# Kernel optimization log

Measured on AMD Instinct MI355X. Metric: run time of the kernel, lower is better.

Reference implementation:

```python
import jax, jax.numpy as jnp
import numpy as np


def setup_inputs() -> dict:
    key = jax.random.key(0)
    k = jax.random.split(key, 5)
    B, L, D = 8, 2048, 256  # D = 2*d_model, c_len == q_len == L (required by source's s1 broadcast)
    c = jax.random.normal(k[0], (B, L, D), dtype=jnp.float32)
    q = jax.random.normal(k[1], (B, L, D), dtype=jnp.float32)
    c_weight = jax.random.normal(k[2], (D, 1), dtype=jnp.float32) * 0.05
    q_weight = jax.random.normal(k[3], (D, 1), dtype=jnp.float32) * 0.05
    cq_weight = jax.random.normal(k[4], (1, 1, D), dtype=jnp.float32) * 0.05
    bias = jnp.zeros((1,), dtype=jnp.float32)
    return {"c": c, "q": q, "c_weight": c_weight, "q_weight": q_weight,
            "cq_weight": cq_weight, "bias": bias}


def reference(c, q, c_weight, q_weight, cq_weight, bias):
    # Dropout omitted (identity) for a deterministic reference.
    # s0: [B, c_len, 1] -> broadcasts over q_len
    s0 = jnp.matmul(c, c_weight)                       # [B, L, 1]
    # s1 (faithful to source, which uses c here): [B, 1, c_len]
    s1 = jnp.swapaxes(jnp.matmul(c, q_weight), 1, 2)   # [B, 1, L]
    # s2: elementwise-scaled batched GEMM: [B, c_len, q_len]
    s2 = jnp.matmul(c * cq_weight, jnp.swapaxes(q, 1, 2))
    s = s0 + s1 + s2 + bias                            # broadcast sum + scalar bias
    return s
```

## Files before the change

kernel.cpp:

```cpp
#include <hip/hip_runtime.h>
#include <hip/hip_bf16.h>

#define B_ 8
#define L_ 2048
#define D_ 256

typedef __bf16 bf16x8 __attribute__((ext_vector_type(8)));
typedef float f32x4 __attribute__((ext_vector_type(4)));

static __device__ __forceinline__ unsigned short f2bf(float f) {
    unsigned int u = __builtin_bit_cast(unsigned int, f);
    unsigned int lsb = (u >> 16) & 1u;
    u += 0x7fffu + lsb;
    return (unsigned short)(u >> 16);
}

static __device__ __forceinline__ void gload_lds16(const void* g, void* l) {
    __builtin_amdgcn_global_load_lds(
        (const __attribute__((address_space(1))) unsigned int*)g,
        (__attribute__((address_space(3))) unsigned int*)l, 16, 0, 0);
}

__global__ __launch_bounds__(256) void prep_kernel(
    const float* __restrict__ c, const float* __restrict__ q,
    const float* __restrict__ cw, const float* __restrict__ qw,
    const float* __restrict__ cqw, const float* __restrict__ bias,
    unsigned short* __restrict__ Abf, unsigned short* __restrict__ Qbf,
    float* __restrict__ s0, float* __restrict__ s1)
{
    const int wave = threadIdx.x >> 6;
    const int lane = threadIdx.x & 63;
    const int row  = blockIdx.x * 4 + wave;

    const float4 cv  = *(const float4*)(c   + (size_t)row * D_ + lane * 4);
    const float4 qv  = *(const float4*)(q   + (size_t)row * D_ + lane * 4);
    const float4 wc  = *(const float4*)(cw  + lane * 4);
    const float4 wq  = *(const float4*)(qw  + lane * 4);
    const float4 wcq = *(const float4*)(cqw + lane * 4);

    ushort4 av, qb;
    av.x = f2bf(cv.x * wcq.x); av.y = f2bf(cv.y * wcq.y);
    av.z = f2bf(cv.z * wcq.z); av.w = f2bf(cv.w * wcq.w);
    qb.x = f2bf(qv.x); qb.y = f2bf(qv.y);
    qb.z = f2bf(qv.z); qb.w = f2bf(qv.w);
    *(ushort4*)(Abf + (size_t)row * D_ + lane * 4) = av;
    *(ushort4*)(Qbf + (size_t)row * D_ + lane * 4) = qb;

    float p0 = cv.x * wc.x + cv.y * wc.y + cv.z * wc.z + cv.w * wc.w;
    float p1 = cv.x * wq.x + cv.y * wq.y + cv.z * wq.z + cv.w * wq.w;
    #pragma unroll
    for (int off = 32; off > 0; off >>= 1) {
        p0 += __shfl_down(p0, off);
        p1 += __shfl_down(p1, off);
    }
    if (lane == 0) { s0[row] = p0 + bias[0]; s1[row] = p1; }
}

#define BM 128
#define BN 128
#define BK 32
#define NSTEP (D_ / BK)

__global__ __launch_bounds__(256) void gemm_kernel(
    const unsigned short* __restrict__ A, const unsigned short* __restrict__ Q,
    const float* __restrict__ s0, const float* __restrict__ s1,
    float* __restrict__ out)
{
    __shared__ __align__(16) unsigned short As[3][BM * BK];
    __shared__ __align__(16) unsigned short Qs[3][BM * BK];

    const int tid  = threadIdx.x;
    const int wave = tid >> 6;
    const int lane = tid & 63;

    const int lin = blockIdx.x + (blockIdx.y << 4) + (blockIdx.z << 8);
    const int nl  = ((lin & 7) << 8) | (lin >> 3);
    const int b   = nl >> 8;
    const int brow = ((nl >> 4) & 15) * BM;
    const int bcol = (nl & 15) * BN;

    const unsigned short* Ab = A + ((size_t)b * L_ + brow) * D_;
    const unsigned short* Qb = Q + ((size_t)b * L_ + bcol) * D_;

    const int wr = wave >> 1;
    const int wc = wave & 1;

    const f32x4 zero = {0.f, 0.f, 0.f, 0.f};
    f32x4 acc[4][4];
    #pragma unroll
    for (int m = 0; m < 4; ++m)
        #pragma unroll
        for (int n = 0; n < 4; ++n) acc[m][n] = zero;

    auto stage = [&](int s) {
        const int k0 = s * BK;
        unsigned short* ab = &As[s % 3][0];
        unsigned short* qb = &Qs[s % 3][0];
        #pragma unroll
        for (int i = 0; i < 2; ++i) {
            const int sidx = i * 256 + wave * 64 + lane;
            const int row  = sidx >> 2;
            const int sl   = sidx & 3;
            const int ksrc = k0 + ((sl ^ ((row >> 1) & 3)) << 3);
            const int wbase = (i * 256 + wave * 64) * 8;
            gload_lds16(Ab + (size_t)row * D_ + ksrc, ab + wbase);
            gload_lds16(Qb + (size_t)row * D_ + ksrc, qb + wbase);
        }
    };

    auto compute = [&](int t) {
        const unsigned short* ab = &As[t % 3][0];
        const unsigned short* qb = &Qs[t % 3][0];
        bf16x8 af[4], qf[4];
        #pragma unroll
        for (int m = 0; m < 4; ++m) {
            const int row = wr * 64 + m * 16 + (lane & 15);
            const int idx = row * 32 + (((lane >> 4) ^ ((row >> 1) & 3)) << 3);
            af[m] = *(const bf16x8*)(ab + idx);
        }
        #pragma unroll
        for (int n = 0; n < 4; ++n) {
            const int row = wc * 64 + n * 16 + (lane & 15);
            const int idx = row * 32 + (((lane >> 4) ^ ((row >> 1) & 3)) << 3);
            qf[n] = *(const bf16x8*)(qb + idx);
        }
        __builtin_amdgcn_s_setprio(1);
        #pragma unroll
        for (int m = 0; m < 4; ++m)
            #pragma unroll
            for (int n = 0; n < 4; ++n)
                acc[m][n] = __builtin_amdgcn_mfma_f32_16x16x32_bf16(
                    af[m], qf[n], acc[m][n], 0, 0, 0);
        __builtin_amdgcn_s_setprio(0);
    };

    stage(0);
    stage(1);

#define STEP(T, VM) do {                                        \
        if ((T) + 2 < NSTEP) stage((T) + 2);                    \
        asm volatile("s_waitcnt vmcnt(" #VM ")" ::: "memory");  \
        __builtin_amdgcn_s_barrier();                           \
        asm volatile("" ::: "memory");                          \
        compute(T);                                             \
        asm volatile("" ::: "memory");                          \
        __builtin_amdgcn_s_barrier();                           \
        asm volatile("" ::: "memory");                          \
    } while (0)

    STEP(0, 8); STEP(1, 8); STEP(2, 8); STEP(3, 8);
    STEP(4, 8); STEP(5, 8); STEP(6, 4); STEP(7, 0);
#undef STEP

    const float* s0b = s0 + b * L_ + brow;
    const float* s1b = s1 + b * L_ + bcol;
    float s1v[4];
    #pragma unroll
    for (int n = 0; n < 4; ++n) s1v[n] = s1b[wc * 64 + n * 16 + (lane & 15)];
    float* outb = out + ((size_t)b * L_ + brow) * L_ + bcol;
    #pragma unroll
    for (int m = 0; m < 4; ++m) {
        #pragma unroll
        for (int r = 0; r < 4; ++r) {
            const int i = wr * 64 + m * 16 + (lane >> 4) * 4 + r;
            const float s0v = s0b[i];
            float* orow = outb + (size_t)i * L_;
            #pragma unroll
            for (int n = 0; n < 4; ++n)
                orow[wc * 64 + n * 16 + (lane & 15)] = acc[m][n][r] + s0v + s1v[n];
        }
    }
}

__global__ void naive_kernel(const float* __restrict__ c, const float* __restrict__ q,
                             const float* __restrict__ cw, const float* __restrict__ qw,
                             const float* __restrict__ cqw, const float* __restrict__ bias,
                             float* __restrict__ out)
{
    const size_t total = (size_t)B_ * L_ * L_;
    for (size_t idx = (size_t)blockIdx.x * blockDim.x + threadIdx.x; idx < total;
         idx += (size_t)gridDim.x * blockDim.x) {
        const int b = (int)(idx / ((size_t)L_ * L_));
        const int rem = (int)(idx % ((size_t)L_ * L_));
        const int i = rem / L_, j = rem % L_;
        const float* ci = c + ((size_t)b * L_ + i) * D_;
        const float* cj = c + ((size_t)b * L_ + j) * D_;
        const float* qj = q + ((size_t)b * L_ + j) * D_;
        float acc = bias[0];
        for (int d = 0; d < D_; ++d)
            acc += ci[d] * cw[d] + cj[d] * qw[d] + ci[d] * cqw[d] * qj[d];
        out[idx] = acc;
    }
}

extern "C" void kernel_launch(void* const* d_in, const int* in_sizes, int n_in,
                              void* d_out, int out_size, void* d_ws, size_t ws_size,
                              hipStream_t stream) {
    const float* c    = (const float*)d_in[0];
    const float* q    = (const float*)d_in[1];
    const float* cw   = (const float*)d_in[2];
    const float* qw   = (const float*)d_in[3];
    const float* cqw  = (const float*)d_in[4];
    const float* bias = (const float*)d_in[5];
    float* out = (float*)d_out;

    const size_t bytesA = (size_t)B_ * L_ * D_ * 2;
    const size_t need   = 2 * bytesA + 2 * (size_t)B_ * L_ * 4;

    if (ws_size >= need) {
        unsigned short* Abf = (unsigned short*)d_ws;
        unsigned short* Qbf = (unsigned short*)((char*)d_ws + bytesA);
        float* s0 = (float*)((char*)d_ws + 2 * bytesA);
        float* s1 = s0 + (size_t)B_ * L_;
        prep_kernel<<<B_ * L_ / 4, 256, 0, stream>>>(c, q, cw, qw, cqw, bias,
                                                     Abf, Qbf, s0, s1);
        dim3 grid(L_ / BN, L_ / BM, B_);
        gemm_kernel<<<grid, 256, 0, stream>>>(Abf, Qbf, s0, s1, out);
    } else {
        naive_kernel<<<2048, 256, 0, stream>>>(c, q, cw, qw, cqw, bias, out);
    }
}
```

Baseline: 47.45 us.

## Enlarge GEMM tile to 256x256 with 512 threads and preload bias into accumulators

Doubles the block tile in both dimensions (256x256, 8 waves, each wave owning a 128x64 sub-tile), which halves global/L2 re-reads of the bf16 operands per output. It switches to a 1D grid of 512 blocks with a batch-interleaving swizzle, and initializes accumulators with s0+s1 so the epilogue is a plain store. The trade-offs are more accumulator registers per thread (128 floats) under a 2-blocks-per-CU launch bound, and fewer blocks for the GPU's CUs, which could cause spills or load imbalance.

```diff
diff --git a/kernel.cpp b/kernel.cpp
--- a/kernel.cpp
+++ b/kernel.cpp
@@ -56,12 +56,12 @@
     if (lane == 0) { s0[row] = p0 + bias[0]; s1[row] = p1; }
 }
 
-#define BM 128
-#define BN 128
+#define BM 256
+#define BN 256
 #define BK 32
 #define NSTEP (D_ / BK)
 
-__global__ __launch_bounds__(256) void gemm_kernel(
+__global__ __launch_bounds__(512, 2) void gemm_kernel(
     const unsigned short* __restrict__ A, const unsigned short* __restrict__ Q,
     const float* __restrict__ s0, const float* __restrict__ s1,
     float* __restrict__ out)
@@ -73,24 +73,37 @@
     const int wave = tid >> 6;
     const int lane = tid & 63;
 
-    const int lin = blockIdx.x + (blockIdx.y << 4) + (blockIdx.z << 8);
-    const int nl  = ((lin & 7) << 8) | (lin >> 3);
-    const int b   = nl >> 8;
-    const int brow = ((nl >> 4) & 15) * BM;
-    const int bcol = (nl & 15) * BN;
+    const int beta = blockIdx.x;
+    const int bs   = ((beta & 7) << 6) | (beta >> 3);
+    const int b    = bs >> 6;
+    const int brow = ((bs >> 3) & 7) * BM;
+    const int bcol = (bs & 7) * BN;
 
     const unsigned short* Ab = A + ((size_t)b * L_ + brow) * D_;
     const unsigned short* Qb = Q + ((size_t)b * L_ + bcol) * D_;
 
-    const int wr = wave >> 1;
-    const int wc = wave & 1;
-
-    const f32x4 zero = {0.f, 0.f, 0.f, 0.f};
-    f32x4 acc[4][4];
-    #pragma unroll
-    for (int m = 0; m < 4; ++m)
-        #pragma unroll
-        for (int n = 0; n < 4; ++n) acc[m][n] = zero;
+    const int wr = wave >> 2;
+    const int wc = wave & 3;
+
+    float s0v[8][4];
+    #pragma unroll
+    for (int m = 0; m < 8; ++m)
+        #pragma unroll
+        for (int r = 0; r < 4; ++r)
+            s0v[m][r] = s0[(size_t)b * L_ + brow + wr * 128 + m * 16 + (lane >> 4) * 4 + r];
+    float s1v[4];
+    #pragma unroll
+    for (int n = 0; n < 4; ++n)
+        s1v[n] = s1[(size_t)b * L_ + bcol + wc * 64 + n * 16 + (lane & 15)];
+
+    f32x4 acc[8][4];
+    #pragma unroll
+    for (int m = 0; m < 8; ++m)
+        #pragma unroll
+        for (int n = 0; n < 4; ++n)
+            #pragma unroll
+            for (int r = 0; r < 4; ++r)
+                acc[m][n][r] = s0v[m][r] + s1v[n];
 
     auto stage = [&](int s) {
         const int k0 = s * BK;
@@ -98,11 +111,11 @@
         unsigned short* qb = &Qs[s % 3][0];
         #pragma unroll
         for (int i = 0; i < 2; ++i) {
-            const int sidx = i * 256 + wave * 64 + lane;
+            const int sidx = i * 512 + wave * 64 + lane;
             const int row  = sidx >> 2;
             const int sl   = sidx & 3;
             const int ksrc = k0 + ((sl ^ ((row >> 1) & 3)) << 3);
-            const int wbase = (i * 256 + wave * 64) * 8;
+            const int wbase = (i * 512 + wave * 64) * 8;
             gload_lds16(Ab + (size_t)row * D_ + ksrc, ab + wbase);
             gload_lds16(Qb + (size_t)row * D_ + ksrc, qb + wbase);
         }
@@ -111,10 +124,10 @@
     auto compute = [&](int t) {
         const unsigned short* ab = &As[t % 3][0];
         const unsigned short* qb = &Qs[t % 3][0];
-        bf16x8 af[4], qf[4];
-        #pragma unroll
-        for (int m = 0; m < 4; ++m) {
-            const int row = wr * 64 + m * 16 + (lane & 15);
+        bf16x8 af[8], qf[4];
+        #pragma unroll
+        for (int m = 0; m < 8; ++m) {
+            const int row = wr * 128 + m * 16 + (lane & 15);
             const int idx = row * 32 + (((lane >> 4) ^ ((row >> 1) & 3)) << 3);
             af[m] = *(const bf16x8*)(ab + idx);
         }
@@ -126,7 +139,7 @@
         }
         __builtin_amdgcn_s_setprio(1);
         #pragma unroll
-        for (int m = 0; m < 4; ++m)
+        for (int m = 0; m < 8; ++m)
             #pragma unroll
             for (int n = 0; n < 4; ++n)
                 acc[m][n] = __builtin_amdgcn_mfma_f32_16x16x32_bf16(
@@ -152,22 +165,16 @@
     STEP(4, 8); STEP(5, 8); STEP(6, 4); STEP(7, 0);
 #undef STEP
 
-    const float* s0b = s0 + b * L_ + brow;
-    const float* s1b = s1 + b * L_ + bcol;
-    float s1v[4];
-    #pragma unroll
-    for (int n = 0; n < 4; ++n) s1v[n] = s1b[wc * 64 + n * 16 + (lane & 15)];
     float* outb = out + ((size_t)b * L_ + brow) * L_ + bcol;
     #pragma unroll
-    for (int m = 0; m < 4; ++m) {
+    for (int m = 0; m < 8; ++m) {
         #pragma unroll
         for (int r = 0; r < 4; ++r) {
-            const int i = wr * 64 + m * 16 + (lane >> 4) * 4 + r;
-            const float s0v = s0b[i];
-            float* orow = outb + (size_t)i * L_;
+            const int row = wr * 128 + m * 16 + (lane >> 4) * 4 + r;
+            float* rp = outb + (size_t)row * L_;
             #pragma unroll
             for (int n = 0; n < 4; ++n)
-                orow[wc * 64 + n * 16 + (lane & 15)] = acc[m][n][r] + s0v + s1v[n];
+                rp[wc * 64 + n * 16 + (lane & 15)] = acc[m][n][r];
         }
     }
 }
@@ -214,8 +221,7 @@
         float* s1 = s0 + (size_t)B_ * L_;
         prep_kernel<<<B_ * L_ / 4, 256, 0, stream>>>(c, q, cw, qw, cqw, bias,
                                                      Abf, Qbf, s0, s1);
-        dim3 grid(L_ / BN, L_ / BM, B_);
-        gemm_kernel<<<grid, 256, 0, stream>>>(Abf, Qbf, s0, s1, out);
+        gemm_kernel<<<dim3(512), 512, 0, stream>>>(Abf, Qbf, s0, s1, out);
     } else {
         naive_kernel<<<2048, 256, 0, stream>>>(c, q, cw, qw, cqw, bias, out);
     }
```

Result: slower. 49.02 us (+3.3%).
